# Optimization experiments

Measured on AMD Instinct MI355X. Metric: run time of the kernel, lower is better.

Reference implementation:

```python
import jax, jax.numpy as jnp
from jax import lax
import numpy as np

CHANNELS = 16
PAD = 2
POOL_K = 3
POOL_S = 2
HIDDEN = 32


def setup_inputs() -> dict:
    key = jax.random.key(0)
    ks = jax.random.split(key, 8)
    N, C, H, W = 64, CHANNELS, 254, 254
    x = jax.random.normal(ks[0], (N, C, H, W), dtype=jnp.float32)
    s_rnn = 1.0 / np.sqrt(HIDDEN)
    s_fc = 1.0 / np.sqrt(HIDDEN)
    W_ih = jax.random.uniform(ks[1], (HIDDEN, CHANNELS), jnp.float32, -s_rnn, s_rnn)
    W_hh = jax.random.uniform(ks[2], (HIDDEN, HIDDEN), jnp.float32, -s_rnn, s_rnn)
    b_ih = jax.random.uniform(ks[3], (HIDDEN,), jnp.float32, -s_rnn, s_rnn)
    b_hh = jax.random.uniform(ks[4], (HIDDEN,), jnp.float32, -s_rnn, s_rnn)
    W_fc = jax.random.uniform(ks[5], (CHANNELS, HIDDEN), jnp.float32, -s_fc, s_fc)
    b_fc = jax.random.uniform(ks[6], (CHANNELS,), jnp.float32, -s_fc, s_fc)
    return {"x": x, "W_ih": W_ih, "W_hh": W_hh, "b_ih": b_ih, "b_hh": b_hh,
            "W_fc": W_fc, "b_fc": b_fc}


def _forward(x, W_ih, W_hh, b_ih, b_hh, W_fc, b_fc):
    # 1. replication pad
    xp = jnp.pad(x, ((0, 0), (0, 0), (PAD, PAD), (PAD, PAD)), mode="edge")
    # 2. L2 pooling: (sum over window of x^2)^(1/2)
    sq = lax.reduce_window(xp * xp, jnp.float32(0.0), lax.add,
                           (1, 1, POOL_K, POOL_K), (1, 1, POOL_S, POOL_S), "VALID")
    pooled = jnp.sqrt(sq)  # (N, C, H_out, W_out)
    N, C, Ho, Wo = pooled.shape
    S = Ho * Wo
    # 3. spatial grid -> sequence (S, N, C)
    seq = pooled.reshape(N, C, S).transpose(2, 0, 1)
    # 4. Elman RNN: precompute input projection, scan over time
    xproj = jnp.einsum("snc,hc->snh", seq, W_ih) + b_ih + b_hh  # (S, N, H)
    h0 = jnp.zeros((N, HIDDEN), dtype=pooled.dtype)

    def step(h, xt):
        h_new = jnp.tanh(xt + h @ W_hh.T)
        return h_new, h_new

    _, rnn_out = lax.scan(step, h0, xproj)  # (S, N, H)
    # 5. linear projection back to channels
    proj = jnp.einsum("snh,ch->snc", rnn_out, W_fc) + b_fc  # (S, N, C)
    # 6. back to grid + residual
    out = proj.transpose(1, 2, 0).reshape(N, C, Ho, Wo) + pooled
    return out


def reference(x, W_ih, W_hh, b_ih, b_hh, W_fc, b_fc):
    return _forward(x, W_ih, W_hh, b_ih, b_hh, W_fc, b_fc)
```

## Files before the change

### kernel.cpp

```cpp
#include <hip/hip_runtime.h>
#include <hip/hip_fp16.h>

#define CH   16
#define HID  32
#define HIN  254
#define WIN  254
#define HO   128
#define WO   128
#define NB   64
#define SLEN (HO * WO)
#define CHUNK 32
#define WARM  16
#define NCHUNK (SLEN / CHUNK)

typedef _Float16 v8h __attribute__((ext_vector_type(8)));
typedef float    v4f __attribute__((ext_vector_type(4)));
typedef float    v2f __attribute__((ext_vector_type(2)));
typedef unsigned int v4u __attribute__((ext_vector_type(4)));
typedef unsigned int v2u __attribute__((ext_vector_type(2)));

__global__ __launch_bounds__(256) void k_pool(const float* __restrict__ x,
                                              _Float16* __restrict__ pooled) {
    const int tid = threadIdx.x;
    const int px  = tid & 63;
    const int wy  = tid >> 6;
    const int y   = blockIdx.x * 4 + wy;
    const int n   = blockIdx.y;

    int r[3];
#pragma unroll
    for (int k = 0; k < 3; ++k) r[k] = min(max(2 * y - 2 + k, 0), HIN - 1);

    const bool left  = (px == 0);
    const bool right = (px == 63);
    const int c0 = left  ? 0   : 4 * px - 2;
    const int c1 = 4 * px;
    const int c2 = right ? 252 : 4 * px + 2;

    const float* xn = x + (size_t)n * CH * HIN * WIN;
    _Float16 ph[2][CH];

#pragma unroll
    for (int cg = 0; cg < 4; ++cg) {
        v2f L[4][3][3];
#pragma unroll
        for (int cc = 0; cc < 4; ++cc) {
            const float* bc = xn + (size_t)(cg * 4 + cc) * HIN * WIN;
#pragma unroll
            for (int k = 0; k < 3; ++k) {
                const float* rp = bc + (size_t)r[k] * WIN;
                L[cc][k][0] = *(const v2f*)(rp + c0);
                L[cc][k][1] = *(const v2f*)(rp + c1);
                L[cc][k][2] = *(const v2f*)(rp + c2);
            }
        }
#pragma unroll
        for (int cc = 0; cc < 4; ++cc) {
            float s0 = 0.f, s1 = 0.f;
#pragma unroll
            for (int k = 0; k < 3; ++k) {
                v2f L0 = L[cc][k][0], L1 = L[cc][k][1], L2 = L[cc][k][2];
                if (left)  L0[1] = L0[0];
                if (right) L2[0] = L2[1];
                s0 += L0[0] * L0[0] + L0[1] * L0[1] + L1[0] * L1[0];
                s1 += L1[0] * L1[0] + L1[1] * L1[1] + L2[0] * L2[0];
            }
            ph[0][cg * 4 + cc] = (_Float16)sqrtf(s0);
            ph[1][cg * 4 + cc] = (_Float16)sqrtf(s1);
        }
    }

    const size_t t = (size_t)y * WO + 2 * px;
    v4u* dst = (v4u*)(pooled + ((size_t)n * SLEN + t) * CH);
    dst[0] = *(const v4u*)&ph[0][0];
    dst[1] = *(const v4u*)&ph[0][8];
    dst[2] = *(const v4u*)&ph[1][0];
    dst[3] = *(const v4u*)&ph[1][8];
}

__global__ __launch_bounds__(256) void k_rnn(const _Float16* __restrict__ pooled,
                                             const float* __restrict__ Wih,
                                             const float* __restrict__ Whh,
                                             const float* __restrict__ bih,
                                             const float* __restrict__ bhh,
                                             const float* __restrict__ Wfc,
                                             const float* __restrict__ bfc,
                                             float* __restrict__ out) {
    const int tid = threadIdx.x;
    const int wid = tid >> 6;
    const int l   = tid & 63;
    const int g   = l >> 4;
    const int q   = l & 15;
    const int rowq = wid * 16 + q;
    const int cid = blockIdx.x;
    const int start = cid * CHUNK;
    const int warm  = min(WARM, start);
    const int t0    = start - warm;

    __shared__ _Float16 hbuf[64][56];
    __shared__ _Float16 sbuf[64][324];

    const float KS = 2.8853900817779268f;

    v8h bWhh[2], bWih[2], bWfc;
#pragma unroll
    for (int nt = 0; nt < 2; ++nt) {
        const float* wr = Whh + (size_t)(nt * 16 + q) * HID + 8 * g;
#pragma unroll
        for (int e = 0; e < 8; ++e) bWhh[nt][e] = (_Float16)(KS * wr[e]);
        const float* wi = Wih + (size_t)(nt * 16 + q) * CH;
#pragma unroll
        for (int e = 0; e < 8; ++e)
            bWih[nt][e] = (g < 2) ? (_Float16)(KS * wi[8 * g + e]) : (_Float16)0.f;
    }
#pragma unroll
    for (int e = 0; e < 8; ++e) bWfc[e] = (_Float16)Wfc[(size_t)q * HID + 8 * g + e];

    float biasH[2];
#pragma unroll
    for (int nt = 0; nt < 2; ++nt)
        biasH[nt] = KS * (bih[nt * 16 + q] + bhh[nt * 16 + q]);
    const float biasC = bfc[q];

    v8h af;
#pragma unroll
    for (int e = 0; e < 8; ++e) af[e] = (_Float16)0.f;

    const _Float16* pb = pooled + (size_t)rowq * SLEN * CH + 4 * g;
    v2u pA = *(const v2u*)(pb + (size_t)t0 * CH);
    v2u pB = *(const v2u*)(pb + (size_t)(t0 + 1) * CH);

    const int aA = (32 * g + q) << 2;
    const int aB = aA + 64;
    const bool glo = (g < 2);

#define RNN_STEP(PRE, TT, EMIT, TTL)                                           \
    {                                                                          \
        const int t = (TT);                                                    \
             \
        *(v2u*)&hbuf[rowq][32 + 4 * g] = PRE;                                  \
                                 \
        unsigned w0 = (unsigned)__builtin_amdgcn_ds_bpermute(aA, (int)PRE[0]); \
        unsigned w1 = (unsigned)__builtin_amdgcn_ds_bpermute(aA, (int)PRE[1]); \
        unsigned w2 = (unsigned)__builtin_amdgcn_ds_bpermute(aB, (int)PRE[0]); \
        unsigned w3 = (unsigned)__builtin_amdgcn_ds_bpermute(aB, (int)PRE[1]); \
        {                                                                      \
            int tn = t + 2; if (tn > SLEN - 1) tn = SLEN - 1;                  \
            PRE = *(const v2u*)(pb + (size_t)tn * CH);                         \
        }                                                                      \
        v4u pfu = { glo ? w0 : 0u, glo ? w1 : 0u,                              \
                    glo ? w2 : 0u, glo ? w3 : 0u };                            \
        v8h pf; __builtin_memcpy(&pf, &pfu, 16);                               \
        v4f acc0, acc1;                                                        \
        {                                                                      \
            v4f ai = {biasH[0], biasH[0], biasH[0], biasH[0]};                 \
            ai = __builtin_amdgcn_mfma_f32_16x16x32_f16(pf, bWih[0], ai, 0, 0, 0); \
            acc0 = __builtin_amdgcn_mfma_f32_16x16x32_f16(af, bWhh[0], ai, 0, 0, 0); \
        }                                                                      \
        {                                                                      \
            v4f ai = {biasH[1], biasH[1], biasH[1], biasH[1]};                 \
            ai = __builtin_amdgcn_mfma_f32_16x16x32_f16(pf, bWih[1], ai, 0, 0, 0); \
            acc1 = __builtin_amdgcn_mfma_f32_16x16x32_f16(af, bWhh[1], ai, 0, 0, 0); \
        }                                                                      \
        _Pragma("unroll")                                                      \
        for (int r = 0; r < 4; ++r) {                                          \
            float e0 = __builtin_amdgcn_exp2f(acc0[r]);                        \
            float e1 = __builtin_amdgcn_exp2f(acc1[r]);                        \
            float h0 = fmaf(-2.f, __builtin_amdgcn_rcpf(e0 + 1.f), 1.f);       \
            float h1 = fmaf(-2.f, __builtin_amdgcn_rcpf(e1 + 1.f), 1.f);       \
            hbuf[wid * 16 + 4 * g + r][q]      = (_Float16)h0;                 \
            hbuf[wid * 16 + 4 * g + r][16 + q] = (_Float16)h1;                 \
        }                                                                      \
        af = *(const v8h*)&hbuf[rowq][8 * g];                                  \
        if (EMIT) {                                                            \
            v4f pj = {biasC, biasC, biasC, biasC};                             \
            pj = __builtin_amdgcn_mfma_f32_16x16x32_f16(af, bWfc, pj, 0, 0, 0);\
            _Pragma("unroll")                                                  \
            for (int r = 0; r < 4; ++r) {                                      \
                const int b = wid * 16 + 4 * g + r;                            \
                float res = (float)hbuf[b][32 + q];                            \
                sbuf[b][q * 20 + (TTL)] = (_Float16)(pj[r] + res);             \
            }                                                                  \
        }                                                                      \
    }

#define FLUSH(TBASE)                                                           \
    {                                                                          \
        _Pragma("unroll")                                                      \
        for (int i = 0; i < 4; ++i) {                                          \
            const int pl = l + 64 * i;                                         \
            const int b  = wid * 16 + (pl >> 4);                               \
            const int c  = pl & 15;                                            \
            const __half2* sp = (const __half2*)&sbuf[b][c * 20];              \
            float* op = out + (size_t)(b * CH + c) * SLEN + (TBASE);           \
            _Pragma("unroll")                                                  \
            for (int j = 0; j < 4; ++j) {                                      \
                float2 f0 = __half22float2(sp[2 * j]);                         \
                float2 f1 = __half22float2(sp[2 * j + 1]);                     \
                v4f v = {f0.x, f0.y, f1.x, f1.y};                              \
                *(v4f*)(op + 4 * j) = v;                                       \
            }                                                                  \
        }                                                                      \
    }

    if (warm) {
#pragma unroll 2
        for (int st = 0; st < WARM; st += 2) {
            RNN_STEP(pA, t0 + st,     0, 0)
            RNN_STEP(pB, t0 + st + 1, 0, 0)
        }
    }
#pragma unroll 2
    for (int st = 0; st < 16; st += 2) {
        RNN_STEP(pA, start + st,     1, st)
        RNN_STEP(pB, start + st + 1, 1, st + 1)
    }
    FLUSH(start)
#pragma unroll 2
    for (int st = 0; st < 16; st += 2) {
        RNN_STEP(pA, start + 16 + st,     1, st)
        RNN_STEP(pB, start + 16 + st + 1, 1, st + 1)
    }
    FLUSH(start + 16)
#undef RNN_STEP
#undef FLUSH
}

__global__ void k_sentinel(float* o) { o[threadIdx.x] = -12345.0f; }

extern "C" void kernel_launch(void* const* d_in, const int* in_sizes, int n_in,
                              void* d_out, int out_size, void* d_ws, size_t ws_size,
                              hipStream_t stream) {
    const float* x   = (const float*)d_in[0];
    const float* Wih = (const float*)d_in[1];
    const float* Whh = (const float*)d_in[2];
    const float* bih = (const float*)d_in[3];
    const float* bhh = (const float*)d_in[4];
    const float* Wfc = (const float*)d_in[5];
    const float* bfc = (const float*)d_in[6];
    float* out = (float*)d_out;

    const size_t poolB = (size_t)NB * SLEN * CH * sizeof(_Float16);
    if (ws_size < poolB) {
        k_sentinel<<<1, 64, 0, stream>>>(out);
        return;
    }
    _Float16* pooled = (_Float16*)d_ws;

    k_pool<<<dim3(HO / 4, NB), 256, 0, stream>>>(x, pooled);
    k_rnn <<<dim3(NCHUNK), 256, 0, stream>>>(pooled, Wih, Whh, bih, bhh, Wfc, bfc, out);
}
```

Before: 122.9 us.

## Halve RNN chunk length and software-pipeline input projection one step ahead

Cuts CHUNK from 32 to 16, which doubles the number of parallel chunk blocks while keeping the 16-step warmup per chunk. The input-projection MFMAs for step t+1 are now issued during step t, so the recurrent dependency chain holds only the Whh MFMA and tanh. The staging buffer layout changes to time-major, a single flush runs at the end, and launch bounds add a minimum-occupancy hint. The trade-off is that redundant warmup work now equals the useful work, since every chunk repeats 16 extra steps.

```diff
diff --git a/kernel.cpp b/kernel.cpp
--- a/kernel.cpp
+++ b/kernel.cpp
@@ -9,7 +9,7 @@
 #define WO   128
 #define NB   64
 #define SLEN (HO * WO)
-#define CHUNK 32
+#define CHUNK 16
 #define WARM  16
 #define NCHUNK (SLEN / CHUNK)
 
@@ -78,14 +78,14 @@
     dst[3] = *(const v4u*)&ph[1][8];
 }
 
-__global__ __launch_bounds__(256) void k_rnn(const _Float16* __restrict__ pooled,
-                                             const float* __restrict__ Wih,
-                                             const float* __restrict__ Whh,
-                                             const float* __restrict__ bih,
-                                             const float* __restrict__ bhh,
-                                             const float* __restrict__ Wfc,
-                                             const float* __restrict__ bfc,
-                                             float* __restrict__ out) {
+__global__ __launch_bounds__(256, 4) void k_rnn(const _Float16* __restrict__ pooled,
+                                                const float* __restrict__ Wih,
+                                                const float* __restrict__ Whh,
+                                                const float* __restrict__ bih,
+                                                const float* __restrict__ bhh,
+                                                const float* __restrict__ Wfc,
+                                                const float* __restrict__ bfc,
+                                                float* __restrict__ out) {
     const int tid = threadIdx.x;
     const int wid = tid >> 6;
     const int l   = tid & 63;
@@ -98,7 +98,7 @@
     const int t0    = start - warm;
 
     __shared__ _Float16 hbuf[64][56];
-    __shared__ _Float16 sbuf[64][324];
+    __shared__ _Float16 sbuf[64][260];
 
     const float KS = 2.8853900817779268f;
 
@@ -116,11 +116,12 @@
 #pragma unroll
     for (int e = 0; e < 8; ++e) bWfc[e] = (_Float16)Wfc[(size_t)q * HID + 8 * g + e];
 
-    float biasH[2];
-#pragma unroll
-    for (int nt = 0; nt < 2; ++nt)
-        biasH[nt] = KS * (bih[nt * 16 + q] + bhh[nt * 16 + q]);
+    float bH0 = KS * (bih[q] + bhh[q]);
+    float bH1 = KS * (bih[16 + q] + bhh[16 + q]);
+    const v4f biasv0 = {bH0, bH0, bH0, bH0};
+    const v4f biasv1 = {bH1, bH1, bH1, bH1};
     const float biasC = bfc[q];
+    const v4f biasCv = {biasC, biasC, biasC, biasC};
 
     v8h af;
 #pragma unroll
@@ -134,34 +135,37 @@
     const int aB = aA + 64;
     const bool glo = (g < 2);
 
-#define RNN_STEP(PRE, TT, EMIT, TTL)                                           \
+    v4f aiA0, aiA1, aiB0, aiB1;
+    {
+        unsigned w0 = (unsigned)__builtin_amdgcn_ds_bpermute(aA, (int)pA[0]);
+        unsigned w1 = (unsigned)__builtin_amdgcn_ds_bpermute(aA, (int)pA[1]);
+        unsigned w2 = (unsigned)__builtin_amdgcn_ds_bpermute(aB, (int)pA[0]);
+        unsigned w3 = (unsigned)__builtin_amdgcn_ds_bpermute(aB, (int)pA[1]);
+        v4u pfu = { glo ? w0 : 0u, glo ? w1 : 0u, glo ? w2 : 0u, glo ? w3 : 0u };
+        v8h pf; __builtin_memcpy(&pf, &pfu, 16);
+        aiA0 = __builtin_amdgcn_mfma_f32_16x16x32_f16(pf, bWih[0], biasv0, 0, 0, 0);
+        aiA1 = __builtin_amdgcn_mfma_f32_16x16x32_f16(pf, bWih[1], biasv1, 0, 0, 0);
+    }
+
+#define RNN_STEP(PC, AI0, AI1, PO, AJ0, AJ1, TT, EMIT, TTL)                    \
     {                                                                          \
         const int t = (TT);                                                    \
-             \
-        *(v2u*)&hbuf[rowq][32 + 4 * g] = PRE;                                  \
-                                 \
-        unsigned w0 = (unsigned)__builtin_amdgcn_ds_bpermute(aA, (int)PRE[0]); \
-        unsigned w1 = (unsigned)__builtin_amdgcn_ds_bpermute(aA, (int)PRE[1]); \
-        unsigned w2 = (unsigned)__builtin_amdgcn_ds_bpermute(aB, (int)PRE[0]); \
-        unsigned w3 = (unsigned)__builtin_amdgcn_ds_bpermute(aB, (int)PRE[1]); \
+        if (EMIT) *(v2u*)&hbuf[rowq][32 + 4 * g] = PC;      \
+        unsigned w0 = (unsigned)__builtin_amdgcn_ds_bpermute(aA, (int)PO[0]);  \
+        unsigned w1 = (unsigned)__builtin_amdgcn_ds_bpermute(aA, (int)PO[1]);  \
+        unsigned w2 = (unsigned)__builtin_amdgcn_ds_bpermute(aB, (int)PO[0]);  \
+        unsigned w3 = (unsigned)__builtin_amdgcn_ds_bpermute(aB, (int)PO[1]);  \
         {                                                                      \
             int tn = t + 2; if (tn > SLEN - 1) tn = SLEN - 1;                  \
-            PRE = *(const v2u*)(pb + (size_t)tn * CH);                         \
+            PC = *(const v2u*)(pb + (size_t)tn * CH);                          \
         }                                                                      \
         v4u pfu = { glo ? w0 : 0u, glo ? w1 : 0u,                              \
                     glo ? w2 : 0u, glo ? w3 : 0u };                            \
         v8h pf; __builtin_memcpy(&pf, &pfu, 16);                               \
-        v4f acc0, acc1;                                                        \
-        {                                                                      \
-            v4f ai = {biasH[0], biasH[0], biasH[0], biasH[0]};                 \
-            ai = __builtin_amdgcn_mfma_f32_16x16x32_f16(pf, bWih[0], ai, 0, 0, 0); \
-            acc0 = __builtin_amdgcn_mfma_f32_16x16x32_f16(af, bWhh[0], ai, 0, 0, 0); \
-        }                                                                      \
-        {                                                                      \
-            v4f ai = {biasH[1], biasH[1], biasH[1], biasH[1]};                 \
-            ai = __builtin_amdgcn_mfma_f32_16x16x32_f16(pf, bWih[1], ai, 0, 0, 0); \
-            acc1 = __builtin_amdgcn_mfma_f32_16x16x32_f16(af, bWhh[1], ai, 0, 0, 0); \
-        }                                                                      \
+        AJ0 = __builtin_amdgcn_mfma_f32_16x16x32_f16(pf, bWih[0], biasv0, 0, 0, 0); \
+        AJ1 = __builtin_amdgcn_mfma_f32_16x16x32_f16(pf, bWih[1], biasv1, 0, 0, 0); \
+        v4f acc0 = __builtin_amdgcn_mfma_f32_16x16x32_f16(af, bWhh[0], AI0, 0, 0, 0); \
+        v4f acc1 = __builtin_amdgcn_mfma_f32_16x16x32_f16(af, bWhh[1], AI1, 0, 0, 0); \
         _Pragma("unroll")                                                      \
         for (int r = 0; r < 4; ++r) {                                          \
             float e0 = __builtin_amdgcn_exp2f(acc0[r]);                        \
@@ -173,57 +177,44 @@
         }                                                                      \
         af = *(const v8h*)&hbuf[rowq][8 * g];                                  \
         if (EMIT) {                                                            \
-            v4f pj = {biasC, biasC, biasC, biasC};                             \
-            pj = __builtin_amdgcn_mfma_f32_16x16x32_f16(af, bWfc, pj, 0, 0, 0);\
+            v4f pj = __builtin_amdgcn_mfma_f32_16x16x32_f16(af, bWfc, biasCv,  \
+                                                            0, 0, 0);          \
             _Pragma("unroll")                                                  \
             for (int r = 0; r < 4; ++r) {                                      \
                 const int b = wid * 16 + 4 * g + r;                            \
                 float res = (float)hbuf[b][32 + q];                            \
-                sbuf[b][q * 20 + (TTL)] = (_Float16)(pj[r] + res);             \
+                sbuf[b][(TTL) * 16 + q] = (_Float16)(pj[r] + res);             \
             }                                                                  \
         }                                                                      \
     }
 
-#define FLUSH(TBASE)                                                           \
-    {                                                                          \
-        _Pragma("unroll")                                                      \
-        for (int i = 0; i < 4; ++i) {                                          \
-            const int pl = l + 64 * i;                                         \
-            const int b  = wid * 16 + (pl >> 4);                               \
-            const int c  = pl & 15;                                            \
-            const __half2* sp = (const __half2*)&sbuf[b][c * 20];              \
-            float* op = out + (size_t)(b * CH + c) * SLEN + (TBASE);           \
-            _Pragma("unroll")                                                  \
-            for (int j = 0; j < 4; ++j) {                                      \
-                float2 f0 = __half22float2(sp[2 * j]);                         \
-                float2 f1 = __half22float2(sp[2 * j + 1]);                     \
-                v4f v = {f0.x, f0.y, f1.x, f1.y};                              \
-                *(v4f*)(op + 4 * j) = v;                                       \
-            }                                                                  \
-        }                                                                      \
-    }
-
-    if (warm) {
 #pragma unroll 2
-        for (int st = 0; st < WARM; st += 2) {
-            RNN_STEP(pA, t0 + st,     0, 0)
-            RNN_STEP(pB, t0 + st + 1, 0, 0)
+    for (int st = 0; st < warm; st += 2) {
+        RNN_STEP(pA, aiA0, aiA1, pB, aiB0, aiB1, t0 + st,     0, 0)
+        RNN_STEP(pB, aiB0, aiB1, pA, aiA0, aiA1, t0 + st + 1, 0, 0)
+    }
+#pragma unroll 2
+    for (int st = 0; st < CHUNK; st += 2) {
+        RNN_STEP(pA, aiA0, aiA1, pB, aiB0, aiB1, start + st,     1, st)
+        RNN_STEP(pB, aiB0, aiB1, pA, aiA0, aiA1, start + st + 1, 1, st + 1)
+    }
+#undef RNN_STEP
+
+#pragma unroll
+    for (int i = 0; i < 4; ++i) {
+        const int pl = l + 64 * i;
+        const int b  = wid * 16 + (pl >> 4);
+        const int c  = pl & 15;
+        float o[16];
+#pragma unroll
+        for (int j = 0; j < 16; ++j) o[j] = (float)sbuf[b][j * 16 + c];
+        float* op = out + (size_t)(b * CH + c) * SLEN + start;
+#pragma unroll
+        for (int j = 0; j < 4; ++j) {
+            v4f v = {o[4 * j], o[4 * j + 1], o[4 * j + 2], o[4 * j + 3]};
+            *(v4f*)(op + 4 * j) = v;
         }
     }
-#pragma unroll 2
-    for (int st = 0; st < 16; st += 2) {
-        RNN_STEP(pA, start + st,     1, st)
-        RNN_STEP(pB, start + st + 1, 1, st + 1)
-    }
-    FLUSH(start)
-#pragma unroll 2
-    for (int st = 0; st < 16; st += 2) {
-        RNN_STEP(pA, start + 16 + st,     1, st)
-        RNN_STEP(pB, start + 16 + st + 1, 1, st + 1)
-    }
-    FLUSH(start + 16)
-#undef RNN_STEP
-#undef FLUSH
 }
 
 __global__ void k_sentinel(float* o) { o[threadIdx.x] = -12345.0f; }
```

Measured after the change: 125.4 us. About the same (+2.0%).

## Restructure pooling kernel to slide row sums and stage output through LDS

Applied to the files above, without the earlier changes.

The pooling kernel now gives each thread one channel and one output column pair, and walks 32 output rows while keeping per-row squared sums in registers. Each input row is therefore read once instead of being reloaded by overlapping pool windows. Results are staged in shared memory and written out as contiguous 16-byte stores in the (n, t, channel) layout. The grid shrinks to 1024 blocks, each doing a serial loop with two barriers per group, which lowers parallelism available for hiding latency.

```diff
diff --git a/kernel.cpp b/kernel.cpp
--- a/kernel.cpp
+++ b/kernel.cpp
@@ -22,60 +22,64 @@
 __global__ __launch_bounds__(256) void k_pool(const float* __restrict__ x,
                                               _Float16* __restrict__ pooled) {
     const int tid = threadIdx.x;
-    const int px  = tid & 63;
-    const int wy  = tid >> 6;
-    const int y   = blockIdx.x * 4 + wy;
-    const int n   = blockIdx.y;
-
-    int r[3];
-#pragma unroll
-    for (int k = 0; k < 3; ++k) r[k] = min(max(2 * y - 2 + k, 0), HIN - 1);
-
-    const bool left  = (px == 0);
-    const bool right = (px == 63);
-    const int c0 = left  ? 0   : 4 * px - 2;
-    const int c1 = 4 * px;
-    const int c2 = right ? 252 : 4 * px + 2;
-
-    const float* xn = x + (size_t)n * CH * HIN * WIN;
-    _Float16 ph[2][CH];
-
-#pragma unroll
-    for (int cg = 0; cg < 4; ++cg) {
-        v2f L[4][3][3];
-#pragma unroll
-        for (int cc = 0; cc < 4; ++cc) {
-            const float* bc = xn + (size_t)(cg * 4 + cc) * HIN * WIN;
-#pragma unroll
-            for (int k = 0; k < 3; ++k) {
-                const float* rp = bc + (size_t)r[k] * WIN;
-                L[cc][k][0] = *(const v2f*)(rp + c0);
-                L[cc][k][1] = *(const v2f*)(rp + c1);
-                L[cc][k][2] = *(const v2f*)(rp + c2);
-            }
+    const int ch  = tid & 15;
+    const int px  = tid >> 4;
+    const int xt  = blockIdx.x;
+    const int ys  = blockIdx.y;
+    const int n   = blockIdx.z;
+    const int p   = xt * 16 + px;
+
+    const bool left  = (p == 0);
+    const bool right = (p == 63);
+    const int c0 = left  ? 0   : 4 * p - 2;
+    const int c1 = 4 * p;
+    const int c2 = right ? 252 : 4 * p + 2;
+
+    const float* base = x + (size_t)(n * CH + ch) * HIN * WIN;
+
+    __shared__ _Float16 st[4][32][16];
+
+    auto rowsum = [&](int rr, float& sA, float& sB) {
+        rr = min(max(rr, 0), HIN - 1);
+        const float* rp = base + (size_t)rr * WIN;
+        v2f L0 = *(const v2f*)(rp + c0);
+        v2f L1 = *(const v2f*)(rp + c1);
+        v2f L2 = *(const v2f*)(rp + c2);
+        if (left)  L0[1] = L0[0];
+        if (right) L2[0] = L2[1];
+        float m = L1[0] * L1[0];
+        sA = fmaf(L0[0], L0[0], fmaf(L0[1], L0[1], m));
+        sB = fmaf(L1[1], L1[1], fmaf(L2[0], L2[0], m));
+    };
+
+    const int ybase = ys * 32;
+    float r0A, r0B, r1A, r1B;
+    rowsum(2 * ybase - 2, r0A, r0B);
+    rowsum(2 * ybase - 1, r1A, r1B);
+
+    for (int grp = 0; grp < 8; ++grp) {
+        const int yg = ybase + grp * 4;
+#pragma unroll
+        for (int yy = 0; yy < 4; ++yy) {
+            const int y = yg + yy;
+            float r2A, r2B, r3A, r3B;
+            rowsum(2 * y,     r2A, r2B);
+            rowsum(2 * y + 1, r3A, r3B);
+            st[yy][2 * px][ch]     = (_Float16)sqrtf(r0A + r1A + r2A);
+            st[yy][2 * px + 1][ch] = (_Float16)sqrtf(r0B + r1B + r2B);
+            r0A = r2A; r0B = r2B; r1A = r3A; r1B = r3B;
         }
-#pragma unroll
-        for (int cc = 0; cc < 4; ++cc) {
-            float s0 = 0.f, s1 = 0.f;
-#pragma unroll
-            for (int k = 0; k < 3; ++k) {
-                v2f L0 = L[cc][k][0], L1 = L[cc][k][1], L2 = L[cc][k][2];
-                if (left)  L0[1] = L0[0];
-                if (right) L2[0] = L2[1];
-                s0 += L0[0] * L0[0] + L0[1] * L0[1] + L1[0] * L1[0];
-                s1 += L1[0] * L1[0] + L1[1] * L1[1] + L2[0] * L2[0];
-            }
-            ph[0][cg * 4 + cc] = (_Float16)sqrtf(s0);
-            ph[1][cg * 4 + cc] = (_Float16)sqrtf(s1);
+        __syncthreads();
+        {
+            const int w = tid >> 6;
+            const int o = tid & 63;
+            const v4u v = *(const v4u*)((const _Float16*)st + (size_t)tid * 8);
+            _Float16* dst = pooled +
+                ((size_t)n * SLEN + (size_t)(yg + w) * WO + xt * 32) * CH + o * 8;
+            *(v4u*)dst = v;
         }
-    }
-
-    const size_t t = (size_t)y * WO + 2 * px;
-    v4u* dst = (v4u*)(pooled + ((size_t)n * SLEN + t) * CH);
-    dst[0] = *(const v4u*)&ph[0][0];
-    dst[1] = *(const v4u*)&ph[0][8];
-    dst[2] = *(const v4u*)&ph[1][0];
-    dst[3] = *(const v4u*)&ph[1][8];
+        __syncthreads();
+    }
 }
 
 __global__ __launch_bounds__(256) void k_rnn(const _Float16* __restrict__ pooled,
@@ -139,7 +143,6 @@
         const int t = (TT);                                                    \
              \
         *(v2u*)&hbuf[rowq][32 + 4 * g] = PRE;                                  \
-                                 \
         unsigned w0 = (unsigned)__builtin_amdgcn_ds_bpermute(aA, (int)PRE[0]); \
         unsigned w1 = (unsigned)__builtin_amdgcn_ds_bpermute(aA, (int)PRE[1]); \
         unsigned w2 = (unsigned)__builtin_amdgcn_ds_bpermute(aB, (int)PRE[0]); \
@@ -247,6 +250,6 @@
     }
     _Float16* pooled = (_Float16*)d_ws;
 
-    k_pool<<<dim3(HO / 4, NB), 256, 0, stream>>>(x, pooled);
+    k_pool<<<dim3(4, 4, NB), 256, 0, stream>>>(x, pooled);
     k_rnn <<<dim3(NCHUNK), 256, 0, stream>>>(pooled, Wih, Whh, bih, bhh, Wfc, bfc, out);
 }
```

Result: slower. 126.2 us (+2.6%).

## Stage pooled inputs through shared-memory tiles with coalesced block-wide prefetch

Applied to the files above, without the earlier changes.

Replaces the per-step 8-byte global load of each row's pooled input with a block-cooperative load of 8 timesteps at a time, issued as 16-byte vector loads into a register staging buffer and then written to a shared-memory tile. The RNN steps read their inputs from LDS, and the next window's global loads overlap the current window's compute. This targets latency and uncoalesced access on the serial recurrence. The cost is two extra __syncthreads per 8 steps, extra LDS usage, and runtime-computed emit and sbuf indices in place of compile-time constants.

```diff
diff --git a/kernel.cpp b/kernel.cpp
--- a/kernel.cpp
+++ b/kernel.cpp
@@ -99,6 +99,7 @@
 
     __shared__ _Float16 hbuf[64][56];
     __shared__ _Float16 sbuf[64][324];
+    __shared__ _Float16 tile[64][9][18];
 
     const float KS = 2.8853900817779268f;
 
@@ -126,28 +127,46 @@
 #pragma unroll
     for (int e = 0; e < 8; ++e) af[e] = (_Float16)0.f;
 
-    const _Float16* pb = pooled + (size_t)rowq * SLEN * CH + 4 * g;
-    v2u pA = *(const v2u*)(pb + (size_t)t0 * CH);
-    v2u pB = *(const v2u*)(pb + (size_t)(t0 + 1) * CH);
-
     const int aA = (32 * g + q) << 2;
     const int aB = aA + 64;
     const bool glo = (g < 2);
 
-#define RNN_STEP(PRE, TT, EMIT, TTL)                                           \
+    const int sn = tid >> 2;
+    const int sp = tid & 3;
+    const _Float16* gsn = pooled + (size_t)sn * SLEN * CH + sp * 8;
+    v4u stg[4];
+
+#define STG_LOAD(TW)                                                           \
+    {                                                                          \
+        const _Float16* s0 = gsn + (size_t)(TW) * CH;                          \
+        stg[0] = *(const v4u*)(s0);                                            \
+        stg[1] = *(const v4u*)(s0 + 32);                                       \
+        stg[2] = *(const v4u*)(s0 + 64);                                       \
+        stg[3] = *(const v4u*)(s0 + 96);                                       \
+    }
+
+#define STG_WRITE()                                                            \
+    {                                                                          \
+        _Pragma("unroll")                                                      \
+        for (int j = 0; j < 4; ++j) {                                          \
+            const int u  = sp + 4 * j;                                         \
+            unsigned* d = (unsigned*)&tile[sn][u >> 1][(u & 1) * 8];           \
+            d[0] = stg[j][0]; d[1] = stg[j][1];                                \
+            d[2] = stg[j][2]; d[3] = stg[j][3];                                \
+        }                                                                      \
+    }
+
+#define RNN_STEP(TL, TT)                                                       \
     {                                                                          \
         const int t = (TT);                                                    \
-             \
-        *(v2u*)&hbuf[rowq][32 + 4 * g] = PRE;                                  \
-                                 \
-        unsigned w0 = (unsigned)__builtin_amdgcn_ds_bpermute(aA, (int)PRE[0]); \
-        unsigned w1 = (unsigned)__builtin_amdgcn_ds_bpermute(aA, (int)PRE[1]); \
-        unsigned w2 = (unsigned)__builtin_amdgcn_ds_bpermute(aB, (int)PRE[0]); \
-        unsigned w3 = (unsigned)__builtin_amdgcn_ds_bpermute(aB, (int)PRE[1]); \
-        {                                                                      \
-            int tn = t + 2; if (tn > SLEN - 1) tn = SLEN - 1;                  \
-            PRE = *(const v2u*)(pb + (size_t)tn * CH);                         \
-        }                                                                      \
+        v2u pp;                                                                \
+        pp[0] = *(const unsigned*)&tile[rowq][TL][4 * g];                      \
+        pp[1] = *(const unsigned*)&tile[rowq][TL][4 * g + 2];                  \
+        *(v2u*)&hbuf[rowq][32 + 4 * g] = pp;                \
+        unsigned w0 = (unsigned)__builtin_amdgcn_ds_bpermute(aA, (int)pp[0]);  \
+        unsigned w1 = (unsigned)__builtin_amdgcn_ds_bpermute(aA, (int)pp[1]);  \
+        unsigned w2 = (unsigned)__builtin_amdgcn_ds_bpermute(aB, (int)pp[0]);  \
+        unsigned w3 = (unsigned)__builtin_amdgcn_ds_bpermute(aB, (int)pp[1]);  \
         v4u pfu = { glo ? w0 : 0u, glo ? w1 : 0u,                              \
                     glo ? w2 : 0u, glo ? w3 : 0u };                            \
         v8h pf; __builtin_memcpy(&pf, &pfu, 16);                               \
@@ -172,14 +191,14 @@
             hbuf[wid * 16 + 4 * g + r][16 + q] = (_Float16)h1;                 \
         }                                                                      \
         af = *(const v8h*)&hbuf[rowq][8 * g];                                  \
-        if (EMIT) {                                                            \
+        if (t >= start) {                                                      \
             v4f pj = {biasC, biasC, biasC, biasC};                             \
             pj = __builtin_amdgcn_mfma_f32_16x16x32_f16(af, bWfc, pj, 0, 0, 0);\
             _Pragma("unroll")                                                  \
             for (int r = 0; r < 4; ++r) {                                      \
                 const int b = wid * 16 + 4 * g + r;                            \
                 float res = (float)hbuf[b][32 + q];                            \
-                sbuf[b][q * 20 + (TTL)] = (_Float16)(pj[r] + res);             \
+                sbuf[b][q * 20 + ((t - start) & 15)] = (_Float16)(pj[r] + res);\
             }                                                                  \
         }                                                                      \
     }
@@ -191,39 +210,49 @@
             const int pl = l + 64 * i;                                         \
             const int b  = wid * 16 + (pl >> 4);                               \
             const int c  = pl & 15;                                            \
-            const __half2* sp = (const __half2*)&sbuf[b][c * 20];              \
+            const __half2* sp2 = (const __half2*)&sbuf[b][c * 20];             \
             float* op = out + (size_t)(b * CH + c) * SLEN + (TBASE);           \
             _Pragma("unroll")                                                  \
             for (int j = 0; j < 4; ++j) {                                      \
-                float2 f0 = __half22float2(sp[2 * j]);                         \
-                float2 f1 = __half22float2(sp[2 * j + 1]);                     \
+                float2 f0 = __half22float2(sp2[2 * j]);                        \
+                float2 f1 = __half22float2(sp2[2 * j + 1]);                    \
                 v4f v = {f0.x, f0.y, f1.x, f1.y};                              \
                 *(v4f*)(op + 4 * j) = v;                                       \
             }                                                                  \
         }                                                                      \
     }
 
-    if (warm) {
-#pragma unroll 2
-        for (int st = 0; st < WARM; st += 2) {
-            RNN_STEP(pA, t0 + st,     0, 0)
-            RNN_STEP(pB, t0 + st + 1, 0, 0)
-        }
-    }
-#pragma unroll 2
-    for (int st = 0; st < 16; st += 2) {
-        RNN_STEP(pA, start + st,     1, st)
-        RNN_STEP(pB, start + st + 1, 1, st + 1)
-    }
-    FLUSH(start)
-#pragma unroll 2
-    for (int st = 0; st < 16; st += 2) {
-        RNN_STEP(pA, start + 16 + st,     1, st)
-        RNN_STEP(pB, start + 16 + st + 1, 1, st + 1)
-    }
-    FLUSH(start + 16)
+    STG_LOAD(t0)
+    STG_WRITE()
+    __syncthreads();
+
+    const int nw = (warm + CHUNK) >> 3;
+    for (int w = 0; w < nw; ++w) {
+        const int tw = t0 + w * 8;
+        const bool more = (w + 1 < nw);
+        if (more) STG_LOAD(tw + 8)
+
+        RNN_STEP(0, tw + 0)
+        RNN_STEP(1, tw + 1)
+        RNN_STEP(2, tw + 2)
+        RNN_STEP(3, tw + 3)
+        RNN_STEP(4, tw + 4)
+        RNN_STEP(5, tw + 5)
+        RNN_STEP(6, tw + 6)
+        RNN_STEP(7, tw + 7)
+
+        const int done = tw + 8 - start;
+        if (done == 16) FLUSH(start)
+        if (done == 32) FLUSH(start + 16)
+
+        __syncthreads();
+        if (more) STG_WRITE();
+        __syncthreads();
+    }
 #undef RNN_STEP
 #undef FLUSH
+#undef STG_LOAD
+#undef STG_WRITE
 }
 
 __global__ void k_sentinel(float* o) { o[threadIdx.x] = -12345.0f; }
```

Measured after the change: 125.7 us. +2.3%, slower.
